# Performance work log

Hardware: AMD Instinct MI355X
Metric: run time of the kernel (lower is better)

Reference implementation:

```python
import jax, jax.numpy as jnp
import numpy as np

NUM_AGES = 100
FEAT_DIM = 512
BATCH = 4096
TEMPERATURE = 0.1
EPS = 1e-6


def setup_inputs() -> dict:
    key = jax.random.key(0)
    k1, k2, k3 = jax.random.split(key, 3)
    z_age = jax.random.normal(k1, (BATCH, FEAT_DIM), dtype=jnp.float32)
    ages = jax.random.randint(k2, (BATCH,), 0, NUM_AGES, dtype=jnp.int64)
    proxies = jax.random.normal(k3, (NUM_AGES, FEAT_DIM), dtype=jnp.float32)
    return {"z_age": z_age, "ages": ages, "proxies": proxies}


def _unit_diff(a, b):
    d = a - b
    return d / (jnp.linalg.norm(d, axis=-1, keepdims=True) + EPS)


def reference(z_age, ages, proxies):
    # Vectorized equivalent of the O(B^2) python double loop.
    # Only pairs with age_i < age_j contribute (age_i > age_j branch is a no-op `...`).
    B = z_age.shape[0]
    A = proxies.shape[0]
    aj = ages.astype(jnp.int32)
    c_cur = proxies[aj]                                   # [B, D]
    c_next = proxies[jnp.minimum(aj + 1, A - 1)]          # [B, D]
    c_prev = proxies[jnp.maximum(aj - 1, 0)]              # [B, D]
    vf = _unit_diff(c_next, c_cur)                        # forward direction per sample j
    vb = _unit_diff(c_prev, c_cur)                        # backward direction per sample j

    # Pairwise norms via Gram matrix: ||z_i - z_j||.
    G = z_age @ z_age.T                                   # [B, B]
    sq = jnp.diagonal(G)                                  # [B]
    d2 = jnp.maximum(sq[:, None] + sq[None, :] - 2.0 * G, 0.0)
    norm = jnp.sqrt(d2)                                   # [B, B]
    denom = norm + EPS

    # dot(v_d_ij, v_f_j) = (z_i . vf_j - z_j . vf_j) / (||z_i - z_j|| + eps)
    Gf = z_age @ vf.T                                     # [B, B], Gf[i, j] = z_i . vf_j
    Gb = z_age @ vb.T
    dot_f = (Gf - jnp.diagonal(Gf)[None, :]) / denom
    dot_b = (Gb - jnp.diagonal(Gb)[None, :]) / denom

    # -log(exp(df/T) / (exp(df/T) + exp(db/T))) = softplus((db - df)/T)
    per_pair = jax.nn.softplus((dot_b - dot_f) / TEMPERATURE)  # [B, B]
    mask = ages[:, None] < ages[None, :]
    loss = jnp.sum(jnp.where(mask, per_pair, 0.0))
    return loss / (B * (B - 1))
```

## Files before the change

### kernel.cpp

```cpp
#include <hip/hip_runtime.h>
#include <hip/hip_bf16.h>

#define NUM_AGES 100
#define FEAT 512
#define BATCH 4096
#define EPSF 1e-6f
#define INV_T 10.0f
#define INV_NORM (1.0f / ((float)BATCH * (float)(BATCH - 1)))

#define BM 128
#define BN 128
#define BK 64
#define NTILES 528

typedef __bf16 bf16_t;
typedef __bf16 v8bf __attribute__((ext_vector_type(8)));
typedef float v4f __attribute__((ext_vector_type(4)));

__device__ __forceinline__ void async16(const void* g, void* l) {
  __builtin_amdgcn_global_load_lds(
      (const __attribute__((address_space(1))) void*)g,
      (__attribute__((address_space(3))) void*)l, 16, 0, 0);
}

__global__ __launch_bounds__(256) void prep_kernel(
    const float* __restrict__ z, const int* __restrict__ ages,
    const float* __restrict__ proxies,
    bf16_t* __restrict__ zb, bf16_t* __restrict__ wb,
    float* __restrict__ sq, float* __restrict__ hd,
    int* __restrict__ ages_s, float* __restrict__ out)
{
  int j = blockIdx.x;
  int t = threadIdx.x;
  if (j == 0 && t == 0) out[0] = 0.0f;

  int araw = ages[j];
  int a = araw < 0 ? 0 : (araw > NUM_AGES - 1 ? NUM_AGES - 1 : araw);
  const float* cc = proxies + (size_t)a * FEAT;
  const float* cn = proxies + (size_t)(a + 1 > NUM_AGES - 1 ? NUM_AGES - 1 : a + 1) * FEAT;
  const float* cp = proxies + (size_t)(a - 1 < 0 ? 0 : a - 1) * FEAT;
  const float* zr = z + (size_t)j * FEAT;

  int cnt = 0;
#pragma unroll
  for (int e = 0; e < BATCH / 256; ++e) {
    int k = t + e * 256;
    int ak = ages[k];
    cnt += (ak < araw || (ak == araw && k < j)) ? 1 : 0;
  }

  int c0 = 2 * t;
  float2 cc2 = *(const float2*)(cc + c0);
  float2 cn2 = *(const float2*)(cn + c0);
  float2 cp2 = *(const float2*)(cp + c0);
  float2 z2  = *(const float2*)(zr + c0);
  float df0 = cn2.x - cc2.x, df1 = cn2.y - cc2.y;
  float db0 = cp2.x - cc2.x, db1 = cp2.y - cc2.y;
  float s_ff = df0 * df0 + df1 * df1;
  float s_bb = db0 * db0 + db1 * db1;
  float s_zz = z2.x * z2.x + z2.y * z2.y;
  float s_zf = z2.x * df0 + z2.y * df1;
  float s_zb = z2.x * db0 + z2.y * db1;

  float fcnt = (float)cnt;
#pragma unroll
  for (int off = 32; off > 0; off >>= 1) {
    s_ff += __shfl_down(s_ff, off, 64);
    s_bb += __shfl_down(s_bb, off, 64);
    s_zz += __shfl_down(s_zz, off, 64);
    s_zf += __shfl_down(s_zf, off, 64);
    s_zb += __shfl_down(s_zb, off, 64);
    fcnt += __shfl_down(fcnt, off, 64);
  }
  __shared__ float red[4][6];
  int wv = t >> 6, lane = t & 63;
  if (lane == 0) {
    red[wv][0] = s_ff; red[wv][1] = s_bb; red[wv][2] = s_zz;
    red[wv][3] = s_zf; red[wv][4] = s_zb; red[wv][5] = fcnt;
  }
  __syncthreads();
  float ff = red[0][0] + red[1][0] + red[2][0] + red[3][0];
  float bb = red[0][1] + red[1][1] + red[2][1] + red[3][1];
  float zz = red[0][2] + red[1][2] + red[2][2] + red[3][2];
  float zdf = red[0][3] + red[1][3] + red[2][3] + red[3][3];
  float zdb = red[0][4] + red[1][4] + red[2][4] + red[3][4];
  int rank = (int)(red[0][5] + red[1][5] + red[2][5] + red[3][5]);

  float rf = 1.0f / (sqrtf(ff) + EPSF);
  float rb = 1.0f / (sqrtf(bb) + EPSF);
  int key = rank & 7;
  int c2s = (c0 & ~63) | (((((c0 >> 3) & 7) ^ key) << 3)) | (c0 & 7);
  float w0 = db0 * rb - df0 * rf;
  float w1 = db1 * rb - df1 * rf;
  union { bf16_t h[2]; unsigned u; } uz, uw;
  uz.h[0] = (bf16_t)z2.x; uz.h[1] = (bf16_t)z2.y;
  uw.h[0] = (bf16_t)w0;   uw.h[1] = (bf16_t)w1;
  *(unsigned*)((char*)zb + ((size_t)rank * FEAT + c2s) * 2) = uz.u;
  *(unsigned*)((char*)wb + ((size_t)rank * FEAT + c2s) * 2) = uw.u;
  if (t == 0) {
    sq[rank] = zz;
    hd[rank] = rb * zdb - rf * zdf;
    ages_s[rank] = araw;
  }
}

__global__ __launch_bounds__(512, 4) void pair_kernel(
    const bf16_t* __restrict__ zb, const bf16_t* __restrict__ wb,
    const float* __restrict__ sq, const float* __restrict__ hd,
    const int* __restrict__ ages, float* __restrict__ out)
{
  __shared__ __attribute__((aligned(16))) char lds[49152];
  __shared__ float s_sqi[BM];
  __shared__ int   s_agei[BM];
  __shared__ float s_sqj[BN];
  __shared__ float s_hdj[BN];
  __shared__ int   s_agej[BN];
  __shared__ float wsum[8];

  int t = threadIdx.x;
  int wv = t >> 6, lane = t & 63;

  int id = (blockIdx.x & 7) * (NTILES / 8) + (blockIdx.x >> 3);
  int bx = 0, rem = id;
  while (rem >= bx + 1) { rem -= bx + 1; ++bx; }
  int by = rem;
  int i0 = by * BM, j0 = bx * BN;

  if (t < BM) {
    s_sqi[t] = sq[i0 + t];
    s_agei[t] = ages[i0 + t];
  } else if (t < BM + BN) {
    int u = t - BM;
    s_sqj[u] = sq[j0 + u];
    s_hdj[u] = hd[j0 + u];
    s_agej[u] = ages[j0 + u];
  }

  v4f accG[4][2], accH[4][2];
#pragma unroll
  for (int a = 0; a < 4; ++a)
#pragma unroll
    for (int b = 0; b < 2; ++b) {
      accG[a][b] = (v4f){0.f, 0.f, 0.f, 0.f};
      accH[a][b] = (v4f){0.f, 0.f, 0.f, 0.f};
    }

  int wm = wv >> 2, wn = wv & 3;
  int lm = lane & 15, q = lane >> 4;
  int psw0 = ((q     ) ^ (lm & 7)) * 16;
  int psw1 = ((q + 4 ) ^ (lm & 7)) * 16;

  int loff = (lane >> 3) * FEAT + (lane & 7) * 8;
  const bf16_t* baseA = zb + (size_t)i0 * FEAT + loff;
  const bf16_t* baseZ = zb + (size_t)j0 * FEAT + loff;
  const bf16_t* baseW = wb + (size_t)j0 * FEAT + loff;

  for (int k0 = 0; k0 < FEAT; k0 += BK) {
#pragma unroll
    for (int c = 0; c < 2; ++c) {
      int chunk = wv * 2 + c;
      async16(baseA + (size_t)chunk * 8 * FEAT + k0, lds + chunk * 1024);
      async16(baseZ + (size_t)chunk * 8 * FEAT + k0, lds + 16384 + chunk * 1024);
      async16(baseW + (size_t)chunk * 8 * FEAT + k0, lds + 32768 + chunk * 1024);
    }
    __syncthreads();

#pragma unroll
    for (int s = 0; s < 2; ++s) {
      int psw = s ? psw1 : psw0;
      v8bf afr[4], bz[2], bw[2];
#pragma unroll
      for (int mi = 0; mi < 4; ++mi) {
        int r = wm * 64 + mi * 16 + lm;
        afr[mi] = *(const v8bf*)(lds + r * 128 + psw);
      }
#pragma unroll
      for (int ni = 0; ni < 2; ++ni) {
        int r = wn * 32 + ni * 16 + lm;
        bz[ni] = *(const v8bf*)(lds + 16384 + r * 128 + psw);
        bw[ni] = *(const v8bf*)(lds + 32768 + r * 128 + psw);
      }
#pragma unroll
      for (int mi = 0; mi < 4; ++mi)
#pragma unroll
        for (int ni = 0; ni < 2; ++ni) {
          accG[mi][ni] = __builtin_amdgcn_mfma_f32_16x16x32_bf16(afr[mi], bz[ni], accG[mi][ni], 0, 0, 0);
          accH[mi][ni] = __builtin_amdgcn_mfma_f32_16x16x32_bf16(afr[mi], bw[ni], accH[mi][ni], 0, 0, 0);
        }
    }
    __syncthreads();
  }

  float tsum = 0.f;
#pragma unroll
  for (int ni = 0; ni < 2; ++ni) {
    int jl = wn * 32 + ni * 16 + lm;
    float sqj = s_sqj[jl];
    float hdj = s_hdj[jl];
    int aj = s_agej[jl];
#pragma unroll
    for (int mi = 0; mi < 4; ++mi) {
#pragma unroll
      for (int r = 0; r < 4; ++r) {
        int il = wm * 64 + mi * 16 + q * 4 + r;
        float g = accG[mi][ni][r];
        float h = accH[mi][ni][r];
        float d2 = fmaxf(s_sqi[il] + sqj - 2.0f * g, 1e-12f);
        float rs = __builtin_amdgcn_rsqf(d2);
        float arg = (h - hdj) * INV_T * rs;
        float sp = fmaxf(arg, 0.0f) + __logf(1.0f + __expf(-fabsf(arg)));
        tsum += (s_agei[il] < aj) ? sp : 0.0f;
      }
    }
  }

#pragma unroll
  for (int off = 32; off > 0; off >>= 1) tsum += __shfl_down(tsum, off, 64);
  if (lane == 0) wsum[wv] = tsum;
  __syncthreads();
  if (t == 0) {
    float bs = 0.f;
#pragma unroll
    for (int w = 0; w < 8; ++w) bs += wsum[w];
    atomicAdd(out, bs * INV_NORM);
  }
}

extern "C" void kernel_launch(void* const* d_in, const int* in_sizes, int n_in,
                              void* d_out, int out_size, void* d_ws, size_t ws_size,
                              hipStream_t stream) {
  const float* z = (const float*)d_in[0];
  const int* ages = (const int*)d_in[1];
  const float* proxies = (const float*)d_in[2];
  float* out = (float*)d_out;

  char* ws = (char*)d_ws;
  bf16_t* zb = (bf16_t*)ws;
  bf16_t* wb = (bf16_t*)(ws + (size_t)4 * 1024 * 1024);
  size_t o = (size_t)8 * 1024 * 1024;
  float* sq      = (float*)(ws + o);
  float* hd      = (float*)(ws + o + 16384);
  int*   ages_s  = (int*)  (ws + o + 32768);

  prep_kernel<<<BATCH, 256, 0, stream>>>(z, ages, proxies, zb, wb, sq, hd, ages_s, out);
  pair_kernel<<<NTILES, 512, 0, stream>>>(zb, wb, sq, hd, ages_s, out);
}
```

Baseline: 105.8 us.

## Process one sample per wavefront in prep kernel with LDS-staged ages

The prep kernel now handles eight samples per 512-thread block, one per wavefront, instead of one sample per 256-thread block. The ages array is staged once into LDS per block, so the rank counting reads from LDS rather than re-reading global memory for every sample. The cross-wave LDS reduction and block barrier are replaced by wave-level xor shuffles. Each lane now does wider float4 loads and 16-byte bf16 stores. The pair kernel is unchanged, so any gain is limited to the prep stage.

Result: faster. 99.23 us (-6.2%).

```diff
diff --git a/kernel.cpp b/kernel.cpp
--- a/kernel.cpp
+++ b/kernel.cpp
@@ -23,83 +23,96 @@
       (__attribute__((address_space(3))) void*)l, 16, 0, 0);
 }
 
-__global__ __launch_bounds__(256) void prep_kernel(
+__global__ __launch_bounds__(512) void prep_kernel(
     const float* __restrict__ z, const int* __restrict__ ages,
     const float* __restrict__ proxies,
     bf16_t* __restrict__ zb, bf16_t* __restrict__ wb,
     float* __restrict__ sq, float* __restrict__ hd,
     int* __restrict__ ages_s, float* __restrict__ out)
 {
-  int j = blockIdx.x;
+  __shared__ __attribute__((aligned(16))) int sa[BATCH];
   int t = threadIdx.x;
-  if (j == 0 && t == 0) out[0] = 0.0f;
-
-  int araw = ages[j];
-  int a = araw < 0 ? 0 : (araw > NUM_AGES - 1 ? NUM_AGES - 1 : araw);
-  const float* cc = proxies + (size_t)a * FEAT;
-  const float* cn = proxies + (size_t)(a + 1 > NUM_AGES - 1 ? NUM_AGES - 1 : a + 1) * FEAT;
-  const float* cp = proxies + (size_t)(a - 1 < 0 ? 0 : a - 1) * FEAT;
-  const float* zr = z + (size_t)j * FEAT;
+  int wv = t >> 6, lane = t & 63;
+  if (blockIdx.x == 0 && t == 0) out[0] = 0.0f;
+
+  ((int4*)sa)[t]       = ((const int4*)ages)[t];
+  ((int4*)sa)[t + 512] = ((const int4*)ages)[t + 512];
+  __syncthreads();
+
+  int j = blockIdx.x * 8 + wv;
+  int araw = sa[j];
 
   int cnt = 0;
-#pragma unroll
-  for (int e = 0; e < BATCH / 256; ++e) {
-    int k = t + e * 256;
-    int ak = ages[k];
-    cnt += (ak < araw || (ak == araw && k < j)) ? 1 : 0;
-  }
-
-  int c0 = 2 * t;
-  float2 cc2 = *(const float2*)(cc + c0);
-  float2 cn2 = *(const float2*)(cn + c0);
-  float2 cp2 = *(const float2*)(cp + c0);
-  float2 z2  = *(const float2*)(zr + c0);
-  float df0 = cn2.x - cc2.x, df1 = cn2.y - cc2.y;
-  float db0 = cp2.x - cc2.x, db1 = cp2.y - cc2.y;
-  float s_ff = df0 * df0 + df1 * df1;
-  float s_bb = db0 * db0 + db1 * db1;
-  float s_zz = z2.x * z2.x + z2.y * z2.y;
-  float s_zf = z2.x * df0 + z2.y * df1;
-  float s_zb = z2.x * db0 + z2.y * db1;
-
-  float fcnt = (float)cnt;
+  const int4* sa4 = (const int4*)sa;
+#pragma unroll
+  for (int e = 0; e < 16; ++e) {
+    int idx = lane + 64 * e;
+    int4 v = sa4[idx];
+    int k = idx * 4;
+    cnt += (v.x < araw || (v.x == araw && k     < j)) ? 1 : 0;
+    cnt += (v.y < araw || (v.y == araw && k + 1 < j)) ? 1 : 0;
+    cnt += (v.z < araw || (v.z == araw && k + 2 < j)) ? 1 : 0;
+    cnt += (v.w < araw || (v.w == araw && k + 3 < j)) ? 1 : 0;
+  }
+
+  int a  = araw < 0 ? 0 : (araw > NUM_AGES - 1 ? NUM_AGES - 1 : araw);
+  int an = a + 1 > NUM_AGES - 1 ? NUM_AGES - 1 : a + 1;
+  int ap = a - 1 < 0 ? 0 : a - 1;
+  int c0 = lane * 8;
+  const float4* cc4 = (const float4*)(proxies + (size_t)a  * FEAT + c0);
+  const float4* cn4 = (const float4*)(proxies + (size_t)an * FEAT + c0);
+  const float4* cp4 = (const float4*)(proxies + (size_t)ap * FEAT + c0);
+  const float4* zr4 = (const float4*)(z + (size_t)j * FEAT + c0);
+
+  float zv[8], df[8], db[8];
+  float ff = 0.f, bb = 0.f, zz = 0.f, zf = 0.f, zbs = 0.f;
+#pragma unroll
+  for (int h = 0; h < 2; ++h) {
+    float4 c4 = cc4[h], n4 = cn4[h], p4 = cp4[h], z4 = zr4[h];
+    float cA[4] = {c4.x, c4.y, c4.z, c4.w};
+    float nA[4] = {n4.x, n4.y, n4.z, n4.w};
+    float pA[4] = {p4.x, p4.y, p4.z, p4.w};
+    float zA[4] = {z4.x, z4.y, z4.z, z4.w};
+#pragma unroll
+    for (int i2 = 0; i2 < 4; ++i2) {
+      int i = h * 4 + i2;
+      zv[i] = zA[i2];
+      df[i] = nA[i2] - cA[i2];
+      db[i] = pA[i2] - cA[i2];
+      ff  += df[i] * df[i];
+      bb  += db[i] * db[i];
+      zz  += zv[i] * zv[i];
+      zf  += zv[i] * df[i];
+      zbs += zv[i] * db[i];
+    }
+  }
+
 #pragma unroll
   for (int off = 32; off > 0; off >>= 1) {
-    s_ff += __shfl_down(s_ff, off, 64);
-    s_bb += __shfl_down(s_bb, off, 64);
-    s_zz += __shfl_down(s_zz, off, 64);
-    s_zf += __shfl_down(s_zf, off, 64);
-    s_zb += __shfl_down(s_zb, off, 64);
-    fcnt += __shfl_down(fcnt, off, 64);
-  }
-  __shared__ float red[4][6];
-  int wv = t >> 6, lane = t & 63;
-  if (lane == 0) {
-    red[wv][0] = s_ff; red[wv][1] = s_bb; red[wv][2] = s_zz;
-    red[wv][3] = s_zf; red[wv][4] = s_zb; red[wv][5] = fcnt;
-  }
-  __syncthreads();
-  float ff = red[0][0] + red[1][0] + red[2][0] + red[3][0];
-  float bb = red[0][1] + red[1][1] + red[2][1] + red[3][1];
-  float zz = red[0][2] + red[1][2] + red[2][2] + red[3][2];
-  float zdf = red[0][3] + red[1][3] + red[2][3] + red[3][3];
-  float zdb = red[0][4] + red[1][4] + red[2][4] + red[3][4];
-  int rank = (int)(red[0][5] + red[1][5] + red[2][5] + red[3][5]);
-
+    ff  += __shfl_xor(ff,  off, 64);
+    bb  += __shfl_xor(bb,  off, 64);
+    zz  += __shfl_xor(zz,  off, 64);
+    zf  += __shfl_xor(zf,  off, 64);
+    zbs += __shfl_xor(zbs, off, 64);
+    cnt += __shfl_xor(cnt, off, 64);
+  }
+  int rank = cnt;
   float rf = 1.0f / (sqrtf(ff) + EPSF);
   float rb = 1.0f / (sqrtf(bb) + EPSF);
   int key = rank & 7;
-  int c2s = (c0 & ~63) | (((((c0 >> 3) & 7) ^ key) << 3)) | (c0 & 7);
-  float w0 = db0 * rb - df0 * rf;
-  float w1 = db1 * rb - df1 * rf;
-  union { bf16_t h[2]; unsigned u; } uz, uw;
-  uz.h[0] = (bf16_t)z2.x; uz.h[1] = (bf16_t)z2.y;
-  uw.h[0] = (bf16_t)w0;   uw.h[1] = (bf16_t)w1;
-  *(unsigned*)((char*)zb + ((size_t)rank * FEAT + c2s) * 2) = uz.u;
-  *(unsigned*)((char*)wb + ((size_t)rank * FEAT + c2s) * 2) = uw.u;
-  if (t == 0) {
+  int c2s = (c0 & ~63) | ((((c0 >> 3) & 7) ^ key) << 3);
+
+  union { bf16_t h[8]; uint4 u; } uz, uw;
+#pragma unroll
+  for (int i = 0; i < 8; ++i) {
+    uz.h[i] = (bf16_t)zv[i];
+    uw.h[i] = (bf16_t)(db[i] * rb - df[i] * rf);
+  }
+  *(uint4*)((char*)zb + ((size_t)rank * FEAT + c2s) * 2) = uz.u;
+  *(uint4*)((char*)wb + ((size_t)rank * FEAT + c2s) * 2) = uw.u;
+  if (lane == 0) {
     sq[rank] = zz;
-    hd[rank] = rb * zdb - rf * zdf;
+    hd[rank] = rb * zbs - rf * zf;
     ages_s[rank] = araw;
   }
 }
@@ -147,8 +160,8 @@
 
   int wm = wv >> 2, wn = wv & 3;
   int lm = lane & 15, q = lane >> 4;
-  int psw0 = ((q     ) ^ (lm & 7)) * 16;
-  int psw1 = ((q + 4 ) ^ (lm & 7)) * 16;
+  int psw0 = ((q    ) ^ (lm & 7)) * 16;
+  int psw1 = ((q + 4) ^ (lm & 7)) * 16;
 
   int loff = (lane >> 3) * FEAT + (lane & 7) * 8;
   const bf16_t* baseA = zb + (size_t)i0 * FEAT + loff;
@@ -242,6 +255,6 @@
   float* hd      = (float*)(ws + o + 16384);
   int*   ages_s  = (int*)  (ws + o + 32768);
 
-  prep_kernel<<<BATCH, 256, 0, stream>>>(z, ages, proxies, zb, wb, sq, hd, ages_s, out);
+  prep_kernel<<<BATCH / 8, 512, 0, stream>>>(z, ages, proxies, zb, wb, sq, hd, ages_s, out);
   pair_kernel<<<NTILES, 512, 0, stream>>>(zb, wb, sq, hd, ages_s, out);
 }
```
